# Kernel optimization log

Measured on AMD Instinct MI355X. Metric: run time of the kernel, lower is better.

Reference implementation:

```python
import jax, jax.numpy as jnp
import numpy as np
from jax import lax

CIN, COUT, NCLS = 512, 256, 1
B, H, W = 4, 64, 64
EPS = 1e-5


def conv1x1(x, w):
    # x: [B,I,H,W], w: [O,I]
    return jnp.einsum('oi,bihw->bohw', w, x)


def conv3x3(x, w):
    # x: [B,I,H,W], w: [O,I,3,3], padding=1
    return lax.conv_general_dilated(x, w, (1, 1), 'SAME',
                                    dimension_numbers=('NCHW', 'OIHW', 'NCHW'))


def bn_relu(x, g, b):
    # training-mode BatchNorm2d (biased var over B,H,W) + ReLU
    mean = jnp.mean(x, axis=(0, 2, 3), keepdims=True)
    var = jnp.var(x, axis=(0, 2, 3), keepdims=True)
    xn = (x - mean) * lax.rsqrt(var + EPS)
    return jax.nn.relu(xn * g[None, :, None, None] + b[None, :, None, None])


def attention(xf, yf, wq, wk, wv, gamma):
    # cross-attn when yf != xf, self-attn when yf is xf; no 1/sqrt(d) scaling (faithful)
    Bb, C, Hh, Ww = xf.shape
    N = Hh * Ww
    q = conv1x1(xf, wq).reshape(Bb, C, N)
    k = conv1x1(yf, wk).reshape(Bb, C, N)
    v = conv1x1(yf, wv).reshape(Bb, C, N)
    att = jax.nn.softmax(jnp.einsum('bcn,bcm->bnm', q, k), axis=-1)  # [B,N,N]
    out = jnp.einsum('bcm,bnm->bcn', v, att).reshape(Bb, C, Hh, Ww)  # v @ att^T
    return gamma * out + xf


def setup_inputs() -> dict:
    key = jax.random.key(0)
    ks = jax.random.split(key, 16)
    Cs = COUT + 2

    def w(k, shape, fan_in):
        return jax.random.normal(k, shape, dtype=jnp.float32) / np.sqrt(fan_in)

    return {
        'x': jax.random.normal(ks[0], (B, CIN, H, W), dtype=jnp.float32),
        'y': jax.random.normal(ks[1], (B, CIN, H, W), dtype=jnp.float32),
        'flow': jax.random.normal(ks[2], (B, 2, H, W), dtype=jnp.float32),
        'w1x1': w(ks[3], (COUT, CIN), CIN),
        'b1x1': jnp.zeros((COUT,), dtype=jnp.float32),
        'ca_wq': w(ks[4], (COUT, COUT), COUT),
        'ca_wk': w(ks[5], (COUT, COUT), COUT),
        'ca_wv': w(ks[6], (COUT, COUT), COUT),
        'ca_gamma': jnp.full((1,), 0.1, dtype=jnp.float32),
        'cbr1_w': w(ks[7], (COUT, COUT, 3, 3), COUT * 9),
        'bn1_g': jnp.ones((COUT,), dtype=jnp.float32),
        'bn1_b': jnp.zeros((COUT,), dtype=jnp.float32),
        'sa_wq': w(ks[8], (Cs, Cs), Cs),
        'sa_wk': w(ks[9], (Cs, Cs), Cs),
        'sa_wv': w(ks[10], (Cs, Cs), Cs),
        'sa_gamma': jnp.full((1,), 0.1, dtype=jnp.float32),
        'cbr2_w': w(ks[11], (COUT, Cs, 3, 3), Cs * 9),
        'bn2_g': jnp.ones((COUT,), dtype=jnp.float32),
        'bn2_b': jnp.zeros((COUT,), dtype=jnp.float32),
        'pred_w': w(ks[12], (NCLS, COUT), COUT),
        'pred_b': jnp.zeros((NCLS,), dtype=jnp.float32),
    }


def reference(x, y, flow, w1x1, b1x1, ca_wq, ca_wk, ca_wv, ca_gamma,
              cbr1_w, bn1_g, bn1_b, sa_wq, sa_wk, sa_wv, sa_gamma,
              cbr2_w, bn2_g, bn2_b, pred_w, pred_b):
    xb = conv1x1(x, w1x1) + b1x1[None, :, None, None]
    yb = conv1x1(y, w1x1) + b1x1[None, :, None, None]
    t = attention(xb, yb, ca_wq, ca_wk, ca_wv, ca_gamma)
    cross_out = bn_relu(conv3x3(t, cbr1_w), bn1_g, bn1_b)
    cat = jnp.concatenate([cross_out, flow], axis=1)  # [B, COUT+2, H, W]
    t = attention(cat, cat, sa_wq, sa_wk, sa_wv, sa_gamma)
    t = bn_relu(conv3x3(t, cbr2_w), bn2_g, bn2_b)
    out = conv1x1(t, pred_w) + pred_b[None, :, None, None]
    return out
```

## Files before the change

### kernel.cpp

```cpp
#include <hip/hip_runtime.h>
#include <hip/hip_bf16.h>
#include <math.h>


#define NPIX 4096
#define NB   4

typedef __attribute__((ext_vector_type(8))) short short8v;
typedef __attribute__((ext_vector_type(4))) float float4v;

__device__ __forceinline__ short f2bs(float f) {
  __hip_bfloat16 h = __float2bfloat16(f);
  short r; __builtin_memcpy(&r, &h, 2); return r;
}

__device__ __forceinline__ void glld16(const void* g, void* l) {
  __builtin_amdgcn_global_load_lds(
      (const __attribute__((address_space(1))) unsigned int*)g,
      (__attribute__((address_space(3))) unsigned int*)l, 16, 0, 0);
}

__device__ __forceinline__ void vbar() { __builtin_amdgcn_s_barrier(); }

__global__ __launch_bounds__(256) void transp_kernel(
    const float* __restrict__ X, __hip_bfloat16* __restrict__ XT)
{
  const int i0 = blockIdx.x * 64, n0 = blockIdx.y * 64, b = blockIdx.z;
  const int tid = threadIdx.x;
  __shared__ float Ls[64][68];
#pragma unroll
  for (int it = 0; it < 4; ++it) {
    int ir = it * 16 + (tid >> 4);
    int nc = (tid & 15) * 4;
    float4 v = *(const float4*)(X + ((size_t)b * 512 + i0 + ir) * NPIX + n0 + nc);
    *(float4*)(&Ls[ir][nc]) = v;
  }
  __syncthreads();
#pragma unroll
  for (int ot = 0; ot < 2; ++ot) {
    int n = ot * 32 + (tid >> 3);
    int ig = tid & 7;
    short8v o;
#pragma unroll
    for (int j = 0; j < 8; ++j) o[j] = f2bs(Ls[8 * ig + j][n]);
    *(short8v*)(XT + ((size_t)b * NPIX + n0 + n) * 512 + i0 + 8 * ig) = o;
  }
}

__global__ void wprep_kernel(const float* __restrict__ Win,
                             __hip_bfloat16* __restrict__ Wout,
                             int Or, int Ir, int Op, int Ip)
{
  size_t total = (size_t)Op * Ip;
  for (size_t e = (size_t)blockIdx.x * 256 + threadIdx.x; e < total;
       e += (size_t)gridDim.x * 256) {
    int i = (int)(e % Ip);
    int o = (int)(e / Ip);
    float v = (o < Or && i < Ir) ? Win[(size_t)o * Ir + i] : 0.f;
    Wout[e] = __float2bfloat16(v);
  }
}

__global__ void wtransbf_kernel(const float* __restrict__ Win,
                                __hip_bfloat16* __restrict__ Wout,
                                int O, int Ir, int Ip)
{
  size_t total = (size_t)9 * O * Ip;
  for (size_t e = (size_t)blockIdx.x * 256 + threadIdx.x; e < total;
       e += (size_t)gridDim.x * 256) {
    int i = (int)(e % Ip);
    size_t r = e / Ip;
    int o = (int)(r % O);
    int dydx = (int)(r / O);
    float v = (i < Ir) ? Win[((size_t)o * Ir + i) * 9 + dydx] : 0.f;
    Wout[e] = __float2bfloat16(v);
  }
}

template<int OMODE>
__global__ __launch_bounds__(256, 3) void gemm3_kernel(
    const __hip_bfloat16* __restrict__ X, const __hip_bfloat16* __restrict__ Wb,
    const float* __restrict__ Bias, float* __restrict__ Yf,
    __hip_bfloat16* __restrict__ Yb, int Ip, int O)
{
  const int n0 = blockIdx.x * 64, o0 = blockIdx.y * 64, b = blockIdx.z;
  const int tid = threadIdx.x, wv = tid >> 6, lane = tid & 63;
  const int lg = lane >> 4, lr = lane & 15;
  __shared__ __align__(16) __hip_bfloat16 Xs[64 * 32];
  __shared__ __align__(16) __hip_bfloat16 Wsh[64 * 32];

  const int nn = tid >> 2, ig = tid & 3;
  const __hip_bfloat16* xrow = X + ((size_t)b * NPIX + n0 + nn) * Ip;
  const __hip_bfloat16* wrow = Wb + (size_t)(o0 + nn) * Ip;
  const int sw = 8 * (ig ^ (nn & 3));

  float4v acc[4];
#pragma unroll
  for (int f = 0; f < 4; ++f) acc[f] = (float4v){0.f, 0.f, 0.f, 0.f};

  const int nch = Ip >> 5;
  short8v xr_ = *(const short8v*)(xrow + sw);
  short8v wr_ = *(const short8v*)(wrow + sw);

  for (int ci = 0; ci < nch; ++ci) {
    __syncthreads();
    *(short8v*)(Xs  + nn * 32 + ig * 8) = xr_;
    *(short8v*)(Wsh + nn * 32 + ig * 8) = wr_;
    __syncthreads();
    if (ci + 1 < nch) {
      xr_ = *(const short8v*)(xrow + (ci + 1) * 32 + sw);
      wr_ = *(const short8v*)(wrow + (ci + 1) * 32 + sw);
    }
    if (OMODE != 4) {
      int ar = 16 * wv + lr;
      short8v a = *(const short8v*)(Xs + ar * 32 + 8 * (lg ^ (ar & 3)));
#pragma unroll
      for (int of = 0; of < 4; ++of) {
        int br = 16 * of + lr;
        short8v bb = *(const short8v*)(Wsh + br * 32 + 8 * (lg ^ (br & 3)));
        acc[of] = __builtin_amdgcn_mfma_f32_16x16x32_bf16(a, bb, acc[of], 0, 0, 0);
      }
    } else {
      int ar = 16 * wv + lr;
      short8v a = *(const short8v*)(Wsh + ar * 32 + 8 * (lg ^ (ar & 3)));
#pragma unroll
      for (int nf = 0; nf < 4; ++nf) {
        int br = 16 * nf + lr;
        short8v bb = *(const short8v*)(Xs + br * 32 + 8 * (lg ^ (br & 3)));
        acc[nf] = __builtin_amdgcn_mfma_f32_16x16x32_bf16(a, bb, acc[nf], 0, 0, 0);
      }
    }
  }

  if (OMODE < 2) {
#pragma unroll
    for (int r = 0; r < 4; ++r) {
      size_t row = (size_t)b * NPIX + n0 + 16 * wv + 4 * lg + r;
#pragma unroll
      for (int of = 0; of < 4; ++of) {
        int o = o0 + 16 * of + lr;
        if (o < O) {
          float v = acc[of][r] + (Bias ? Bias[o] : 0.f);
          if (OMODE == 0) Yf[row * O + o] = v;
          Yb[row * O + o] = __float2bfloat16(v);
        }
      }
    }
  } else if (OMODE == 3) {
    __hip_bfloat16* Hb = Yb + (size_t)b * NPIX * O;
#pragma unroll
    for (int r = 0; r < 4; ++r) {
      size_t n = n0 + 16 * wv + 4 * lg + r;
#pragma unroll
      for (int of = 0; of < 4; ++of) {
        int o = o0 + 16 * of + lr;
        if (o < O)
          Hb[((size_t)(o >> 3) * NPIX + n) * 8 + (o & 7)] = __float2bfloat16(acc[of][r]);
      }
    }
  } else {
    __hip_bfloat16* Hb = Yb + (size_t)b * NPIX * O;
#pragma unroll
    for (int r = 0; r < 4; ++r) {
      int c = o0 + 16 * wv + 4 * lg + r;
      if (c < O) {
#pragma unroll
        for (int nf = 0; nf < 4; ++nf) {
          int n = n0 + 16 * nf + lr;
          Hb[((size_t)(n >> 3) * O + c) * 8 + (n & 7)] = __float2bfloat16(acc[nf][r]);
        }
      }
    }
  }
}

template<int C, int RF, int S>
__global__ __launch_bounds__(256, 2) void flash4_kernel(
    const __hip_bfloat16* __restrict__ Q, const __hip_bfloat16* __restrict__ K,
    const __hip_bfloat16* __restrict__ V,
    __hip_bfloat16* __restrict__ Opart, float* __restrict__ ml)
{
  constexpr int N    = NPIX;
  constexpr int NC32 = C / 32;
  constexpr int NCF  = C / 16;
  constexpr int QB   = 16 * RF;
// ... 86 lines not shown
          rs += p;
          Ps[(size_t)(w * QB + 16 * rf + 4 * lg + r) * 72 + 16 * mf + lr] =
              __float2bfloat16(p);
        }
#pragma unroll
        for (int off = 1; off < 16; off <<= 1) rs += __shfl_xor(rs, off);
        lrun[rf][r] = lrun[rf][r] * sc + rs;
        scal[rf][r] = sc;
      }
#pragma unroll
    for (int rf = 0; rf < RF; ++rf)
#pragma unroll
      for (int f = 0; f < NCF; ++f)
#pragma unroll
        for (int r = 0; r < 4; ++r) oacc[rf][f][r] *= scal[rf][r];

    asm volatile("s_waitcnt lgkmcnt(0)" ::: "memory");

    short8v pa[RF][2];
#pragma unroll
    for (int rf = 0; rf < RF; ++rf)
#pragma unroll
      for (int h = 0; h < 2; ++h)
        pa[rf][h] = *(const short8v*)(Ps + (size_t)(w * QB + 16 * rf + lr) * 72 +
                                      32 * h + 8 * lg);
    __builtin_amdgcn_s_setprio(1);
#pragma unroll
    for (int cf = 0; cf < NCF; ++cf)
#pragma unroll
      for (int h = 0; h < 2; ++h) {
        short8v vf = *(const short8v*)(Vs + ((h * 4 + lg) * C + 16 * cf + lr) * 8);
#pragma unroll
        for (int rf = 0; rf < RF; ++rf)
          oacc[rf][cf] =
              __builtin_amdgcn_mfma_f32_16x16x32_bf16(pa[rf][h], vf, oacc[rf][cf], 0, 0, 0);
      }
    __builtin_amdgcn_s_setprio(0);
  }

  const size_t rbase = (size_t)(split * NB + b) * N;
#pragma unroll
  for (int rf = 0; rf < RF; ++rf)
#pragma unroll
    for (int r = 0; r < 4; ++r) {
      int n = n0 + QB * w + 16 * rf + 4 * lg + r;
      if (lr == 0) {
        ml[(rbase + n) * 2]     = mrun[rf][r];
        ml[(rbase + n) * 2 + 1] = lrun[rf][r];
      }
#pragma unroll
      for (int cf = 0; cf < NCF; ++cf)
        Opart[(rbase + n) * C + 16 * cf + lr] = __float2bfloat16(oacc[rf][cf][r]);
    }
}

template<int C, int S>
__global__ __launch_bounds__(256) void merge4_kernel(
    const __hip_bfloat16* __restrict__ Op, const float* __restrict__ ml,
    const float* __restrict__ R, const float* __restrict__ gamma_p,
    __hip_bfloat16* __restrict__ T)
{
  const size_t row = blockIdx.x;
  float m = -INFINITY;
#pragma unroll
  for (int s = 0; s < S; ++s)
    m = fmaxf(m, ml[((size_t)s * NB * NPIX + row) * 2]);
  float e[S]; float L = 0.f;
#pragma unroll
  for (int s = 0; s < S; ++s) {
    e[s] = __expf(ml[((size_t)s * NB * NPIX + row) * 2] - m);
    L += ml[((size_t)s * NB * NPIX + row) * 2 + 1] * e[s];
  }
  float rinv = gamma_p[0] / L;
  for (int c = threadIdx.x; c < C; c += 256) {
    float o = 0.f;
#pragma unroll
    for (int s = 0; s < S; ++s)
      o += __bfloat162float(Op[((size_t)s * NB * NPIX + row) * C + c]) * e[s];
    T[row * C + c] = __float2bfloat16(o * rinv + R[row * C + c]);
  }
}

template<int IC>
__global__ __launch_bounds__(256, 1) void conv5_kernel(
    const __hip_bfloat16* __restrict__ X, const __hip_bfloat16* __restrict__ W2,
    float* __restrict__ Y)
{
  constexpr int NCH = IC / 32;
  constexpr int XP = 66 * 32;
  const int h0 = blockIdx.x * 4, o0 = blockIdx.y * 64, b = blockIdx.z;
  const int tid = threadIdx.x, wv = tid >> 6, lane = tid & 63;
  const int lg = lane >> 4, lr = lane & 15;

  __shared__ __align__(1024) __hip_bfloat16 Xs[2][6 * XP];
  __shared__ __align__(1024) __hip_bfloat16 Wsh[2][9 * 2048];

  const __hip_bfloat16 zz = __float2bfloat16(0.f);
  for (int e = tid; e < 384; e += 256) {
    int p = e / 64, side = (e >> 5) & 1, ch = e & 31;
    int sl = side ? 65 : 0;
    Xs[0][p * XP + sl * 32 + ch] = zz;
    Xs[1][p * XP + sl * 32 + ch] = zz;
  }
#pragma unroll
  for (int p = 0; p < 6; ++p) {
    int hs = h0 - 1 + p;
// ... 11 lines not shown
  for (int pf = 0; pf < 4; ++pf)
#pragma unroll
    for (int of = 0; of < 4; ++of) acc[pf][of] = (float4v){0.f, 0.f, 0.f, 0.f};

#define CSTAGE(BUF, CI)                                                        \
  _Pragma("unroll")                                                            \
  for (int k = 0; k < 6; ++k) {                                                \
    int j = wv + k * 4;                                                        \
    int p = j >> 2, seg = j & 3;                                               \
    int hs = h0 - 1 + p;                                                       \
    if (hs >= 0 && hs < 64) {                                                  \
      int px = seg * 16 + (lane >> 2), ig = lane & 3;                          \
      int sl = px + 1;                                                         \
      glld16(X + ((size_t)(b * NPIX + hs * 64 + px)) * IC + (CI) * 32 +        \
                 8 * (ig ^ (sl & 3)),                                          \
             &Xs[BUF][p * XP + (1 + seg * 16) * 32]);                          \
    }                                                                          \
  }                                                                            \
  _Pragma("unroll")                                                            \
  for (int k = 0; k < 9; ++k) {                                                \
    int j = wv + k * 4;                                                        \
    int dydx = j >> 2, seg = j & 3;                                            \
    int oo = seg * 16 + (lane >> 2), ig = lane & 3;                            \
    glld16(W2 + ((size_t)(dydx * 256 + o0 + oo)) * IC + (CI) * 32 +            \
               8 * (ig ^ (oo & 3)),                                            \
           &Wsh[BUF][dydx * 2048 + seg * 512]);                                \
  }

  CSTAGE(0, 0);
  int cur = 0;
  for (int ci = 0; ci < NCH; ++ci) {
    asm volatile("s_waitcnt vmcnt(0) lgkmcnt(0)" ::: "memory");
    vbar();
    __builtin_amdgcn_sched_barrier(0);
    const int cn = (ci + 1 == NCH) ? 0 : ci + 1;
    if (cur) { CSTAGE(0, cn); } else { CSTAGE(1, cn); }
    const __hip_bfloat16* xb = &Xs[cur][0];
    const __hip_bfloat16* wb = &Wsh[cur][0];
    __builtin_amdgcn_s_setprio(1);
#pragma unroll
    for (int dy = 0; dy < 3; ++dy) {
      const __hip_bfloat16* xpl = xb + (wv + dy) * XP;
#pragma unroll
      for (int dx = 0; dx < 3; ++dx) {
        short8v a[4];
#pragma unroll
        for (int pf = 0; pf < 4; ++pf) {
          int sl = pf * 16 + lr + dx;
          a[pf] = *(const short8v*)(xpl + sl * 32 + 8 * (lg ^ (sl & 3)));
        }
#pragma unroll
        for (int of = 0; of < 4; ++of) {
          int br = 16 * of + lr;
          short8v bb = *(const short8v*)(wb + (dy * 3 + dx) * 2048 + br * 32 +
                                         8 * (lg ^ (br & 3)));
#pragma unroll
          for (int pf = 0; pf < 4; ++pf)
            acc[pf][of] = __builtin_amdgcn_mfma_f32_16x16x32_bf16(a[pf], bb,
                                                                  acc[pf][of], 0, 0, 0);
        }
      }
    }
    __builtin_amdgcn_s_setprio(0);
    cur ^= 1;
  }
#undef CSTAGE

#pragma unroll
  for (int pf = 0; pf < 4; ++pf)
#pragma unroll
    for (int r = 0; r < 4; ++r) {
      size_t row = (size_t)b * NPIX + (h0 + wv) * 64 + 16 * pf + 4 * lg + r;
#pragma unroll
      for (int of = 0; of < 4; ++of)
        Y[row * 256 + o0 + 16 * of + lr] = acc[pf][of][r];
    }
}

__global__ __launch_bounds__(256) void stats1_kernel(
    const float* __restrict__ X, float* __restrict__ Part)
{
  const int o0 = (blockIdx.x & 3) * 64;
  const int rc = blockIdx.x >> 2;
  const int tid = threadIdx.x;
  const int o = o0 + (tid & 63), rq = tid >> 6;
  float s = 0.f, sq = 0.f;
  for (int rr = rq; rr < 256; rr += 4) {
    float v = X[(size_t)(rc * 256 + rr) * 256 + o];
    s += v; sq += v * v;
  }
  __shared__ float rs[256], rq2[256];
  rs[tid] = s; rq2[tid] = sq;
  __syncthreads();
  if (tid < 64) {
    s  = rs[tid] + rs[tid + 64] + rs[tid + 128] + rs[tid + 192];
    sq = rq2[tid] + rq2[tid + 64] + rq2[tid + 128] + rq2[tid + 192];
    Part[(o0 + tid) * 128 + rc * 2]     = s;
    Part[(o0 + tid) * 128 + rc * 2 + 1] = sq;
  }
}

__global__ __launch_bounds__(256) void stats2_kernel(
    const float* __restrict__ Part, float* __restrict__ Mean, float* __restrict__ Rstd)
{
  const int o = threadIdx.x;
  float s = 0.f, sq = 0.f;
  for (int rc = 0; rc < 64; ++rc) {
    s += Part[o * 128 + rc * 2];
    sq += Part[o * 128 + rc * 2 + 1];
  }
  float mean = s / 16384.f;
  float var = sq / 16384.f - mean * mean;
  Mean[o] = mean;
  Rstd[o] = 1.f / sqrtf(var + 1e-5f);
}

__global__ __launch_bounds__(320) void bnapply1_kernel(
    const float* __restrict__ X, const float* __restrict__ Flow,
    const float* __restrict__ Mean, const float* __restrict__ Rstd,
    const float* __restrict__ G, const float* __restrict__ Bt,
    float* __restrict__ CatF, __hip_bfloat16* __restrict__ CatB)
{
  const size_t row = blockIdx.x;
  const int t = threadIdx.x;
  if (t >= 288) return;
  float val;
  if (t < 256) {
    float v = X[row * 256 + t];
    val = fmaxf((v - Mean[t]) * Rstd[t] * G[t] + Bt[t], 0.f);
  } else if (t < 258) {
    int b = (int)(row >> 12), n = (int)(row & 4095);
    val = Flow[((size_t)(b * 2 + (t - 256)) << 12) + n];
  } else val = 0.f;
  CatF[row * 288 + t] = val;
  CatB[row * 288 + t] = __float2bfloat16(val);
}

__global__ __launch_bounds__(256) void bnapply2_kernel(
    float* X, const float* __restrict__ Mean, const float* __restrict__ Rstd,
    const float* __restrict__ G, const float* __restrict__ Bt)
{
  const size_t idx = (size_t)blockIdx.x * 256 + threadIdx.x;
  const int t = threadIdx.x;
  float v = X[idx];
  X[idx] = fmaxf((v - Mean[t]) * Rstd[t] * G[t] + Bt[t], 0.f);
}

__global__ __launch_bounds__(256) void pred3_kernel(
    const float* __restrict__ X, const float* __restrict__ Wp,
    const float* __restrict__ Bp, float* __restrict__ Out)
{
  const int wv = threadIdx.x >> 6, lane = threadIdx.x & 63;
  const size_t row = (size_t)blockIdx.x * 4 + wv;
  const float* xr = X + row * 256;
  float acc = 0.f;
#pragma unroll
  for (int cc = 0; cc < 4; ++cc) acc = fmaf(xr[cc * 64 + lane], Wp[cc * 64 + lane], acc);
#pragma unroll
  for (int off = 1; off < 64; off <<= 1) acc += __shfl_xor(acc, off);
  if (lane == 0) Out[row] = acc + Bp[0];
}

extern "C" void kernel_launch(void* const* d_in, const int* in_sizes, int n_in,
                              void* d_out, int out_size, void* d_ws, size_t ws_size,
                              hipStream_t stream)
{
  (void)in_sizes; (void)n_in; (void)out_size; (void)ws_size;
  const float* x      = (const float*)d_in[0];
  const float* y      = (const float*)d_in[1];
  const float* flow   = (const float*)d_in[2];
  const float* w1x1   = (const float*)d_in[3];
  const float* b1x1   = (const float*)d_in[4];
  const float* ca_wq  = (const float*)d_in[5];
  const float* ca_wk  = (const float*)d_in[6];
  const float* ca_wv  = (const float*)d_in[7];
  const float* ca_g   = (const float*)d_in[8];
  const float* cbr1_w = (const float*)d_in[9];
  const float* bn1_g  = (const float*)d_in[10];
  const float* bn1_b  = (const float*)d_in[11];
  const float* sa_wq  = (const float*)d_in[12];
  const float* sa_wk  = (const float*)d_in[13];
  const float* sa_wv  = (const float*)d_in[14];
  const float* sa_g   = (const float*)d_in[15];
  const float* cbr2_w = (const float*)d_in[16];
  const float* bn2_g  = (const float*)d_in[17];
  const float* bn2_b  = (const float*)d_in[18];
  const float* pred_w = (const float*)d_in[19];
  const float* pred_b = (const float*)d_in[20];
  float* out = (float*)d_out;

  const size_t FSZ = (size_t)NB * NPIX * 288;
  const size_t SSZ = FSZ / 2;
  float* ws = (float*)d_ws;
  float* F0 = ws;
  float* F1 = ws + FSZ;
  float* F2 = ws + 2 * FSZ;
  float* Sb = ws + 3 * FSZ;
  __hip_bfloat16* S0 = (__hip_bfloat16*)(Sb);
  __hip_bfloat16* S1 = (__hip_bfloat16*)(Sb + SSZ);
  __hip_bfloat16* S2 = (__hip_bfloat16*)(Sb + 2 * SSZ);
  __hip_bfloat16* S3 = (__hip_bfloat16*)(Sb + 3 * SSZ);
  __hip_bfloat16* S4 = (__hip_bfloat16*)(Sb + 4 * SSZ);
  float* Wr = Sb + 5 * SSZ;
  __hip_bfloat16* w1bf  = (__hip_bfloat16*)Wr;
  __hip_bfloat16* caqb  = w1bf + (size_t)256 * 512;
  __hip_bfloat16* cakb  = caqb + (size_t)256 * 256;
  __hip_bfloat16* cavb  = cakb + (size_t)256 * 256;
  __hip_bfloat16* saqb  = cavb + (size_t)256 * 256;
  __hip_bfloat16* sakb  = saqb + (size_t)320 * 288;
  __hip_bfloat16* savb  = sakb + (size_t)320 * 288;
  __hip_bfloat16* w2abf = savb + (size_t)320 * 288;
  __hip_bfloat16* w2bbf = w2abf + (size_t)9 * 256 * 256;
  float* Part = (float*)(w2bbf + (size_t)9 * 256 * 288);
  float* Mean = Part + 32768;
  float* Rstd = Mean + 256;
  float* Mlb  = Rstd + 256;

  __hip_bfloat16* xT = (__hip_bfloat16*)F0;
  __hip_bfloat16* yT = (__hip_bfloat16*)F1;
  __hip_bfloat16* Op = (__hip_bfloat16*)F0;

  dim3 blk(256);

  wprep_kernel<<<dim3(256), blk, 0, stream>>>(w1x1, w1bf, 256, 512, 256, 512);
  wprep_kernel<<<dim3(256), blk, 0, stream>>>(ca_wq, caqb, 256, 256, 256, 256);
  wprep_kernel<<<dim3(256), blk, 0, stream>>>(ca_wk, cakb, 256, 256, 256, 256);
  wprep_kernel<<<dim3(256), blk, 0, stream>>>(ca_wv, cavb, 256, 256, 256, 256);
  wprep_kernel<<<dim3(256), blk, 0, stream>>>(sa_wq, saqb, 258, 258, 320, 288);
  wprep_kernel<<<dim3(256), blk, 0, stream>>>(sa_wk, sakb, 258, 258, 320, 288);
  wprep_kernel<<<dim3(256), blk, 0, stream>>>(sa_wv, savb, 258, 258, 320, 288);
  wtransbf_kernel<<<dim3(512), blk, 0, stream>>>(cbr1_w, w2abf, 256, 256, 256);
  wtransbf_kernel<<<dim3(512), blk, 0, stream>>>(cbr2_w, w2bbf, 256, 258, 288);

  transp_kernel<<<dim3(8, 64, 4), blk, 0, stream>>>(x, xT);
  transp_kernel<<<dim3(8, 64, 4), blk, 0, stream>>>(y, yT);

  gemm3_kernel<0><<<dim3(64, 4, 4), blk, 0, stream>>>(xT, w1bf, b1x1, F2, S0, 512, 256);
  gemm3_kernel<1><<<dim3(64, 4, 4), blk, 0, stream>>>(yT, w1bf, b1x1, nullptr, S1, 512, 256);

  gemm3_kernel<1><<<dim3(64, 4, 4), blk, 0, stream>>>(S0, caqb, nullptr, nullptr, S2, 256, 256);
  gemm3_kernel<3><<<dim3(64, 4, 4), blk, 0, stream>>>(S1, cakb, nullptr, nullptr, S3, 256, 256);
  gemm3_kernel<4><<<dim3(64, 4, 4), blk, 0, stream>>>(S1, cavb, nullptr, nullptr, S4, 256, 256);

  flash4_kernel<256, 2, 4><<<dim3(32, 4, 4), blk, 0, stream>>>(S2, S3, S4, Op, Mlb);
  merge4_kernel<256, 4><<<dim3(16384), blk, 0, stream>>>(Op, Mlb, F2, ca_g, S0);

  conv5_kernel<256><<<dim3(16, 4, 4), blk, 0, stream>>>(S0, w2abf, F0);
  stats1_kernel<<<dim3(256), blk, 0, stream>>>(F0, Part);
  stats2_kernel<<<dim3(1), blk, 0, stream>>>(Part, Mean, Rstd);
  bnapply1_kernel<<<dim3(16384), dim3(320), 0, stream>>>(F0, flow, Mean, Rstd,
                                                         bn1_g, bn1_b, F1, S3);

  gemm3_kernel<1><<<dim3(64, 5, 4), blk, 0, stream>>>(S3, saqb, nullptr, nullptr, S0, 288, 288);
  gemm3_kernel<3><<<dim3(64, 5, 4), blk, 0, stream>>>(S3, sakb, nullptr, nullptr, S1, 288, 288);
  gemm3_kernel<4><<<dim3(64, 5, 4), blk, 0, stream>>>(S3, savb, nullptr, nullptr, S2, 288, 288);

  flash4_kernel<288, 1, 2><<<dim3(64, 2, 4), blk, 0, stream>>>(S0, S1, S2, Op, Mlb);
  merge4_kernel<288, 2><<<dim3(16384), blk, 0, stream>>>(Op, Mlb, F1, sa_g, S4);

  conv5_kernel<288><<<dim3(16, 4, 4), blk, 0, stream>>>(S4, w2bbf, F0);
  stats1_kernel<<<dim3(256), blk, 0, stream>>>(F0, Part);
  stats2_kernel<<<dim3(1), blk, 0, stream>>>(Part, Mean, Rstd);
  bnapply2_kernel<<<dim3(16384), blk, 0, stream>>>(F0, Mean, Rstd, bn2_g, bn2_b);

  pred3_kernel<<<dim3(4096), blk, 0, stream>>>(F0, pred_w, pred_b, out);
}
```

Before: 530.9 us.

## Merge prep launches, double-buffer gemm loads, add split-4 self-attention flash kernel

The nine weight-prep launches become one 2D-grid kernel, and the two input transposes become one launch. The 1x1 GEMM now stages tiles straight into double-buffered LDS with global_load_lds instead of a register round trip, aiming to overlap loads with MFMA. Self-attention uses a new flash6 kernel with a 4-way KV split and one 16-row tile per wave, which skips the rescale when the running max moves by less than 8, plus a 4-way merge. The bnapply1 output buffer moves from F1 to F2, which adds extra Op/ml partial traffic and risks an aliasing mistake if F2 is still needed.

```diff
diff --git a/kernel.cpp b/kernel.cpp
--- a/kernel.cpp
+++ b/kernel.cpp
@@ -23,16 +23,20 @@
 __device__ __forceinline__ void vbar() { __builtin_amdgcn_s_barrier(); }
 
 __global__ __launch_bounds__(256) void transp_kernel(
-    const float* __restrict__ X, __hip_bfloat16* __restrict__ XT)
-{
-  const int i0 = blockIdx.x * 64, n0 = blockIdx.y * 64, b = blockIdx.z;
+    const float* __restrict__ X, const float* __restrict__ Y,
+    __hip_bfloat16* __restrict__ XT, __hip_bfloat16* __restrict__ YT)
+{
+  const int i0 = blockIdx.x * 64, n0 = blockIdx.y * 64;
+  const int z = blockIdx.z, b = z & 3;
+  const float* S = (z < 4) ? X : Y;
+  __hip_bfloat16* D = (z < 4) ? XT : YT;
   const int tid = threadIdx.x;
   __shared__ float Ls[64][68];
 #pragma unroll
   for (int it = 0; it < 4; ++it) {
     int ir = it * 16 + (tid >> 4);
     int nc = (tid & 15) * 4;
-    float4 v = *(const float4*)(X + ((size_t)b * 512 + i0 + ir) * NPIX + n0 + nc);
+    float4 v = *(const float4*)(S + ((size_t)b * 512 + i0 + ir) * NPIX + n0 + nc);
     *(float4*)(&Ls[ir][nc]) = v;
   }
   __syncthreads();
@@ -43,37 +47,55 @@
     short8v o;
 #pragma unroll
     for (int j = 0; j < 8; ++j) o[j] = f2bs(Ls[8 * ig + j][n]);
-    *(short8v*)(XT + ((size_t)b * NPIX + n0 + n) * 512 + i0 + 8 * ig) = o;
-  }
-}
-
-__global__ void wprep_kernel(const float* __restrict__ Win,
-                             __hip_bfloat16* __restrict__ Wout,
-                             int Or, int Ir, int Op, int Ip)
-{
-  size_t total = (size_t)Op * Ip;
-  for (size_t e = (size_t)blockIdx.x * 256 + threadIdx.x; e < total;
-       e += (size_t)gridDim.x * 256) {
-    int i = (int)(e % Ip);
-    int o = (int)(e / Ip);
-    float v = (o < Or && i < Ir) ? Win[(size_t)o * Ir + i] : 0.f;
-    Wout[e] = __float2bfloat16(v);
-  }
-}
-
-__global__ void wtransbf_kernel(const float* __restrict__ Win,
-                                __hip_bfloat16* __restrict__ Wout,
-                                int O, int Ir, int Ip)
-{
-  size_t total = (size_t)9 * O * Ip;
-  for (size_t e = (size_t)blockIdx.x * 256 + threadIdx.x; e < total;
-       e += (size_t)gridDim.x * 256) {
-    int i = (int)(e % Ip);
-    size_t r = e / Ip;
-    int o = (int)(r % O);
-    int dydx = (int)(r / O);
-    float v = (i < Ir) ? Win[((size_t)o * Ir + i) * 9 + dydx] : 0.f;
-    Wout[e] = __float2bfloat16(v);
+    *(short8v*)(D + ((size_t)b * NPIX + n0 + n) * 512 + i0 + 8 * ig) = o;
+  }
+}
+
+__global__ void wprep_all(
+    const float* __restrict__ w1, const float* __restrict__ cq,
+    const float* __restrict__ ck, const float* __restrict__ cv,
+    const float* __restrict__ sq, const float* __restrict__ sk,
+    const float* __restrict__ sv, const float* __restrict__ c1,
+    const float* __restrict__ c2,
+    __hip_bfloat16* __restrict__ w1o, __hip_bfloat16* __restrict__ cqo,
+    __hip_bfloat16* __restrict__ cko, __hip_bfloat16* __restrict__ cvo,
+    __hip_bfloat16* __restrict__ sqo, __hip_bfloat16* __restrict__ sko,
+    __hip_bfloat16* __restrict__ svo, __hip_bfloat16* __restrict__ c1o,
+    __hip_bfloat16* __restrict__ c2o)
+{
+  const int seg = blockIdx.y;
+  const float* src; __hip_bfloat16* dst;
+  int Or, Ir, Op, Ip, isconv = 0;
+  switch (seg) {
+    case 0: src = w1; dst = w1o; Or = 256; Ir = 512; Op = 256; Ip = 512; break;
+    case 1: src = cq; dst = cqo; Or = 256; Ir = 256; Op = 256; Ip = 256; break;
+    case 2: src = ck; dst = cko; Or = 256; Ir = 256; Op = 256; Ip = 256; break;
+    case 3: src = cv; dst = cvo; Or = 256; Ir = 256; Op = 256; Ip = 256; break;
+    case 4: src = sq; dst = sqo; Or = 258; Ir = 258; Op = 320; Ip = 288; break;
+    case 5: src = sk; dst = sko; Or = 258; Ir = 258; Op = 320; Ip = 288; break;
+    case 6: src = sv; dst = svo; Or = 258; Ir = 258; Op = 320; Ip = 288; break;
+    case 7: src = c1; dst = c1o; Or = 256; Ir = 256; Op = 256; Ip = 256; isconv = 1; break;
+    default: src = c2; dst = c2o; Or = 256; Ir = 258; Op = 256; Ip = 288; isconv = 1; break;
+  }
+  if (!isconv) {
+    size_t total = (size_t)Op * Ip;
+    for (size_t e = (size_t)blockIdx.x * 256 + threadIdx.x; e < total;
+         e += (size_t)gridDim.x * 256) {
+      int i = (int)(e % Ip), o = (int)(e / Ip);
+      float v = (o < Or && i < Ir) ? src[(size_t)o * Ir + i] : 0.f;
+      dst[e] = __float2bfloat16(v);
+    }
+  } else {
+    size_t total = (size_t)9 * Op * Ip;
+    for (size_t e = (size_t)blockIdx.x * 256 + threadIdx.x; e < total;
+         e += (size_t)gridDim.x * 256) {
+      int i = (int)(e % Ip);
+      size_t r = e / Ip;
+      int o = (int)(r % Op);
+      int dydx = (int)(r / Op);
+      float v = (i < Ir) ? src[((size_t)o * Ir + i) * 9 + dydx] : 0.f;
+      dst[e] = __float2bfloat16(v);
+    }
   }
 }
 
@@ -86,51 +108,55 @@
   const int n0 = blockIdx.x * 64, o0 = blockIdx.y * 64, b = blockIdx.z;
   const int tid = threadIdx.x, wv = tid >> 6, lane = tid & 63;
   const int lg = lane >> 4, lr = lane & 15;
-  __shared__ __align__(16) __hip_bfloat16 Xs[64 * 32];
-  __shared__ __align__(16) __hip_bfloat16 Wsh[64 * 32];
+  __shared__ __align__(1024) __hip_bfloat16 Xs[2][64 * 32];
+  __shared__ __align__(1024) __hip_bfloat16 Wsh[2][64 * 32];
 
   const int nn = tid >> 2, ig = tid & 3;
-  const __hip_bfloat16* xrow = X + ((size_t)b * NPIX + n0 + nn) * Ip;
-  const __hip_bfloat16* wrow = Wb + (size_t)(o0 + nn) * Ip;
-  const int sw = 8 * (ig ^ (nn & 3));
+  const __hip_bfloat16* xsrc = X + ((size_t)b * NPIX + n0 + nn) * Ip + 8 * (ig ^ (nn & 3));
+  const __hip_bfloat16* wsrc = Wb + (size_t)(o0 + nn) * Ip + 8 * (ig ^ (nn & 3));
 
   float4v acc[4];
 #pragma unroll
   for (int f = 0; f < 4; ++f) acc[f] = (float4v){0.f, 0.f, 0.f, 0.f};
 
   const int nch = Ip >> 5;
-  short8v xr_ = *(const short8v*)(xrow + sw);
-  short8v wr_ = *(const short8v*)(wrow + sw);
-
+
+#define GSTAGE(BUF, CI)                            \
+  glld16(xsrc + (CI) * 32, &Xs[BUF][tid * 8]);     \
+  glld16(wsrc + (CI) * 32, &Wsh[BUF][tid * 8]);
+
+  GSTAGE(0, 0);
+  int cur = 0;
   for (int ci = 0; ci < nch; ++ci) {
-    __syncthreads();
-    *(short8v*)(Xs  + nn * 32 + ig * 8) = xr_;
-    *(short8v*)(Wsh + nn * 32 + ig * 8) = wr_;
+    asm volatile("s_waitcnt vmcnt(0)" ::: "memory");
     __syncthreads();
     if (ci + 1 < nch) {
-      xr_ = *(const short8v*)(xrow + (ci + 1) * 32 + sw);
-      wr_ = *(const short8v*)(wrow + (ci + 1) * 32 + sw);
-    }
+      if (cur) { GSTAGE(0, ci + 1); } else { GSTAGE(1, ci + 1); }
+    }
+    const __hip_bfloat16* xb = &Xs[cur][0];
+    const __hip_bfloat16* wb = &Wsh[cur][0];
     if (OMODE != 4) {
       int ar = 16 * wv + lr;
-      short8v a = *(const short8v*)(Xs + ar * 32 + 8 * (lg ^ (ar & 3)));
+      short8v a = *(const short8v*)(xb + ar * 32 + 8 * (lg ^ (ar & 3)));
 #pragma unroll
       for (int of = 0; of < 4; ++of) {
         int br = 16 * of + lr;
-        short8v bb = *(const short8v*)(Wsh + br * 32 + 8 * (lg ^ (br & 3)));
-        acc[of] = __builtin_amdgcn_mfma_f32_16x16x32_bf16(a, bb, acc[of], 0, 0, 0);
+        short8v bbv = *(const short8v*)(wb + br * 32 + 8 * (lg ^ (br & 3)));
+        acc[of] = __builtin_amdgcn_mfma_f32_16x16x32_bf16(a, bbv, acc[of], 0, 0, 0);
       }
     } else {
       int ar = 16 * wv + lr;
-      short8v a = *(const short8v*)(Wsh + ar * 32 + 8 * (lg ^ (ar & 3)));
+      short8v a = *(const short8v*)(wb + ar * 32 + 8 * (lg ^ (ar & 3)));
 #pragma unroll
       for (int nf = 0; nf < 4; ++nf) {
         int br = 16 * nf + lr;
-        short8v bb = *(const short8v*)(Xs + br * 32 + 8 * (lg ^ (br & 3)));
-        acc[nf] = __builtin_amdgcn_mfma_f32_16x16x32_bf16(a, bb, acc[nf], 0, 0, 0);
-      }
-    }
-  }
+        short8v bbv = *(const short8v*)(xb + br * 32 + 8 * (lg ^ (br & 3)));
+        acc[nf] = __builtin_amdgcn_mfma_f32_16x16x32_bf16(a, bbv, acc[nf], 0, 0, 0);
+      }
+    }
+    cur ^= 1;
+  }
+#undef GSTAGE
 
   if (OMODE < 2) {
 #pragma unroll
@@ -323,6 +349,152 @@
       for (int cf = 0; cf < NCF; ++cf)
         Opart[(rbase + n) * C + 16 * cf + lr] = __float2bfloat16(oacc[rf][cf][r]);
     }
+}
+
+template<int C, int S>
+__global__ __launch_bounds__(256, 3) void flash6_kernel(
+    const __hip_bfloat16* __restrict__ Q, const __hip_bfloat16* __restrict__ K,
+    const __hip_bfloat16* __restrict__ V,
+    __hip_bfloat16* __restrict__ Opart, float* __restrict__ ml)
+{
+  constexpr int N    = NPIX;
+  constexpr int NC32 = C / 32;
+  constexpr int NCF  = C / 16;
+  constexpr int KBYTES = (C / 8) * 32 * 8 * 2;
+  constexpr int NINST = C / 16;
+  constexpr int NT   = (N / S) / 32;
+
+  __shared__ __align__(1024) char smem[2 * KBYTES];
+  __hip_bfloat16* Ks = (__hip_bfloat16*)smem;
+  __hip_bfloat16* Vs = (__hip_bfloat16*)(smem + KBYTES);
+  __hip_bfloat16* Ps = (__hip_bfloat16*)smem;
+
+  const int n0 = blockIdx.x * 64;
+  const int split = blockIdx.y, b = blockIdx.z;
+  const int tid = threadIdx.x, w = tid >> 6, lane = tid & 63;
+  const int lg = lane >> 4, lr = lane & 15;
+
+  const __hip_bfloat16* Kb = K + (size_t)b * N * C;
+  const __hip_bfloat16* Vb = V + (size_t)b * N * C;
+
+  short8v qf[NC32];
+  {
+    const __hip_bfloat16* qp = Q + ((size_t)b * N + n0 + 16 * w + lr) * C + 8 * lg;
+#pragma unroll
+    for (int ks = 0; ks < NC32; ++ks) qf[ks] = *(const short8v*)(qp + 32 * ks);
+  }
+
+  float4v oacc[NCF];
+#pragma unroll
+  for (int f = 0; f < NCF; ++f) oacc[f] = (float4v){0.f, 0.f, 0.f, 0.f};
+  float mrun[4], lrun[4];
+#pragma unroll
+  for (int r = 0; r < 4; ++r) { mrun[r] = -INFINITY; lrun[r] = 0.f; }
+
+  const int m0base = split * (N / S);
+
+  for (int t = 0; t < NT; ++t) {
+    const int m0 = m0base + t * 32;
+    __syncthreads();
+    for (int u = w; u < NINST; u += 4)
+      glld16(Kb + ((size_t)(2 * u + (lane >> 5)) * N + m0 + (lane & 31)) * 8,
+             Ks + u * 512);
+    for (int u = w; u < NINST; u += 4) {
+      int s = u * 64 + lane;
+      int kv8 = s / C, c = s % C;
+      glld16(Vb + ((size_t)(m0 / 8 + kv8) * C + c) * 8, Vs + s * 8);
+    }
+    asm volatile("s_waitcnt vmcnt(0)" ::: "memory");
+    __syncthreads();
+
+    float4v sacc[2];
+#pragma unroll
+    for (int mf = 0; mf < 2; ++mf) sacc[mf] = (float4v){0.f, 0.f, 0.f, 0.f};
+    __builtin_amdgcn_s_setprio(1);
+#pragma unroll
+    for (int ks = 0; ks < NC32; ++ks)
+#pragma unroll
+      for (int mf = 0; mf < 2; ++mf) {
+        short8v kf = *(const short8v*)(Ks + ((4 * ks + lg) * 32 + 16 * mf + lr) * 8);
+        sacc[mf] = __builtin_amdgcn_mfma_f32_16x16x32_bf16(qf[ks], kf, sacc[mf], 0, 0, 0);
+      }
+    __builtin_amdgcn_s_setprio(0);
+    __syncthreads();
+
+    float pm[4];
+#pragma unroll
+    for (int r = 0; r < 4; ++r) {
+      float p = fmaxf(sacc[0][r], sacc[1][r]);
+#pragma unroll
+      for (int off = 1; off < 16; off <<= 1) p = fmaxf(p, __shfl_xor(p, off));
+      pm[r] = p;
+    }
+    int myok = 1;
+#pragma unroll
+    for (int r = 0; r < 4; ++r) myok &= (pm[r] <= mrun[r] + 8.f) ? 1 : 0;
+    if (__all(myok)) {
+#pragma unroll
+      for (int r = 0; r < 4; ++r) {
+        float rs = 0.f;
+#pragma unroll
+        for (int mf = 0; mf < 2; ++mf) {
+          float p = __expf(sacc[mf][r] - mrun[r]);
+          rs += p;
+          Ps[(16 * w + 4 * lg + r) * 40 + 16 * mf + lr] = __float2bfloat16(p);
+        }
+#pragma unroll
+        for (int off = 1; off < 16; off <<= 1) rs += __shfl_xor(rs, off);
+        lrun[r] += rs;
+      }
+    } else {
+      float scal[4];
+#pragma unroll
+      for (int r = 0; r < 4; ++r) {
+        float mnew = fmaxf(mrun[r], pm[r]);
+        float sc = __expf(mrun[r] - mnew);
+        mrun[r] = mnew;
+        float rs = 0.f;
+#pragma unroll
+        for (int mf = 0; mf < 2; ++mf) {
+          float p = __expf(sacc[mf][r] - mnew);
+          rs += p;
+          Ps[(16 * w + 4 * lg + r) * 40 + 16 * mf + lr] = __float2bfloat16(p);
+        }
+#pragma unroll
+        for (int off = 1; off < 16; off <<= 1) rs += __shfl_xor(rs, off);
+        lrun[r] = lrun[r] * sc + rs;
+        scal[r] = sc;
+      }
+#pragma unroll
+      for (int f = 0; f < NCF; ++f)
+#pragma unroll
+        for (int r = 0; r < 4; ++r) oacc[f][r] *= scal[r];
+    }
+
+    asm volatile("s_waitcnt lgkmcnt(0)" ::: "memory");
+
+    short8v pa = *(const short8v*)(Ps + (16 * w + lr) * 40 + 8 * lg);
+    __builtin_amdgcn_s_setprio(1);
+#pragma unroll
+    for (int cf = 0; cf < NCF; ++cf) {
+      short8v vf = *(const short8v*)(Vs + (lg * C + 16 * cf + lr) * 8);
+      oacc[cf] = __builtin_amdgcn_mfma_f32_16x16x32_bf16(pa, vf, oacc[cf], 0, 0, 0);
+    }
+    __builtin_amdgcn_s_setprio(0);
+  }
+
+  const size_t rbase = (size_t)(split * NB + b) * N;
+#pragma unroll
+  for (int r = 0; r < 4; ++r) {
+    int n = n0 + 16 * w + 4 * lg + r;
+    if (lr == 0) {
+      ml[(rbase + n) * 2]     = mrun[r];
+      ml[(rbase + n) * 2 + 1] = lrun[r];
+    }
+#pragma unroll
+    for (int cf = 0; cf < NCF; ++cf)
+      Opart[(rbase + n) * C + 16 * cf + lr] = __float2bfloat16(oacc[cf][r]);
+  }
 }
 
 template<int C, int S>
@@ -440,11 +612,11 @@
 #pragma unroll
         for (int of = 0; of < 4; ++of) {
           int br = 16 * of + lr;
-          short8v bb = *(const short8v*)(wb + (dy * 3 + dx) * 2048 + br * 32 +
-                                         8 * (lg ^ (br & 3)));
+          short8v bbv = *(const short8v*)(wb + (dy * 3 + dx) * 2048 + br * 32 +
+                                          8 * (lg ^ (br & 3)));
 #pragma unroll
           for (int pf = 0; pf < 4; ++pf)
-            acc[pf][of] = __builtin_amdgcn_mfma_f32_16x16x32_bf16(a[pf], bb,
+            acc[pf][of] = __builtin_amdgcn_mfma_f32_16x16x32_bf16(a[pf], bbv,
                                                                   acc[pf][of], 0, 0, 0);
         }
       }
@@ -610,18 +782,11 @@
 
   dim3 blk(256);
 
-  wprep_kernel<<<dim3(256), blk, 0, stream>>>(w1x1, w1bf, 256, 512, 256, 512);
-  wprep_kernel<<<dim3(256), blk, 0, stream>>>(ca_wq, caqb, 256, 256, 256, 256);
-  wprep_kernel<<<dim3(256), blk, 0, stream>>>(ca_wk, cakb, 256, 256, 256, 256);
-  wprep_kernel<<<dim3(256), blk, 0, stream>>>(ca_wv, cavb, 256, 256, 256, 256);
-  wprep_kernel<<<dim3(256), blk, 0, stream>>>(sa_wq, saqb, 258, 258, 320, 288);
-  wprep_kernel<<<dim3(256), blk, 0, stream>>>(sa_wk, sakb, 258, 258, 320, 288);
-  wprep_kernel<<<dim3(256), blk, 0, stream>>>(sa_wv, savb, 258, 258, 320, 288);
-  wtransbf_kernel<<<dim3(512), blk, 0, stream>>>(cbr1_w, w2abf, 256, 256, 256);
-  wtransbf_kernel<<<dim3(512), blk, 0, stream>>>(cbr2_w, w2bbf, 256, 258, 288);
-
-  transp_kernel<<<dim3(8, 64, 4), blk, 0, stream>>>(x, xT);
-  transp_kernel<<<dim3(8, 64, 4), blk, 0, stream>>>(y, yT);
+  wprep_all<<<dim3(48, 9), blk, 0, stream>>>(
+      w1x1, ca_wq, ca_wk, ca_wv, sa_wq, sa_wk, sa_wv, cbr1_w, cbr2_w,
+      w1bf, caqb, cakb, cavb, saqb, sakb, savb, w2abf, w2bbf);
+
+  transp_kernel<<<dim3(8, 64, 8), blk, 0, stream>>>(x, y, xT, yT);
 
   gemm3_kernel<0><<<dim3(64, 4, 4), blk, 0, stream>>>(xT, w1bf, b1x1, F2, S0, 512, 256);
   gemm3_kernel<1><<<dim3(64, 4, 4), blk, 0, stream>>>(yT, w1bf, b1x1, nullptr, S1, 512, 256);
@@ -637,14 +802,14 @@
   stats1_kernel<<<dim3(256), blk, 0, stream>>>(F0, Part);
   stats2_kernel<<<dim3(1), blk, 0, stream>>>(Part, Mean, Rstd);
   bnapply1_kernel<<<dim3(16384), dim3(320), 0, stream>>>(F0, flow, Mean, Rstd,
-                                                         bn1_g, bn1_b, F1, S3);
+                                                         bn1_g, bn1_b, F2, S3);
 
   gemm3_kernel<1><<<dim3(64, 5, 4), blk, 0, stream>>>(S3, saqb, nullptr, nullptr, S0, 288, 288);
   gemm3_kernel<3><<<dim3(64, 5, 4), blk, 0, stream>>>(S3, sakb, nullptr, nullptr, S1, 288, 288);
   gemm3_kernel<4><<<dim3(64, 5, 4), blk, 0, stream>>>(S3, savb, nullptr, nullptr, S2, 288, 288);
 
-  flash4_kernel<288, 1, 2><<<dim3(64, 2, 4), blk, 0, stream>>>(S0, S1, S2, Op, Mlb);
-  merge4_kernel<288, 2><<<dim3(16384), blk, 0, stream>>>(Op, Mlb, F1, sa_g, S4);
+  flash6_kernel<288, 4><<<dim3(64, 4, 4), blk, 0, stream>>>(S0, S1, S2, Op, Mlb);
+  merge4_kernel<288, 4><<<dim3(16384), blk, 0, stream>>>(Op, Mlb, F2, sa_g, S4);
 
   conv5_kernel<288><<<dim3(16, 4, 4), blk, 0, stream>>>(S4, w2bbf, F0);
   stats1_kernel<<<dim3(256), blk, 0, stream>>>(F0, Part);
```

New measurement: 986.9 us. 1.86x slower.

## Batch weight prep, merge transposes, double-buffer GEMM loads, fuse BN2 into predictor

Applied to the files above, without the earlier changes.

Nine weight-conversion launches become one kernel indexed by blockIdx.y, and the two input transposes become one launch. The 1x1 GEMM switches from register staging to double-buffered global_load_lds direct-to-LDS copies, which cuts one barrier per chunk. The final BN+ReLU pass is fused into the prediction dot product, removing a full read/write sweep of the 16 MB conv output. Buffer F1 is renamed to F2 for the concatenated features. The new GEMM keeps the same swizzle but relies on vmcnt waits for correctness.

```diff
diff --git a/kernel.cpp b/kernel.cpp
--- a/kernel.cpp
+++ b/kernel.cpp
@@ -23,16 +23,20 @@
 __device__ __forceinline__ void vbar() { __builtin_amdgcn_s_barrier(); }
 
 __global__ __launch_bounds__(256) void transp_kernel(
-    const float* __restrict__ X, __hip_bfloat16* __restrict__ XT)
-{
-  const int i0 = blockIdx.x * 64, n0 = blockIdx.y * 64, b = blockIdx.z;
+    const float* __restrict__ X, const float* __restrict__ Y,
+    __hip_bfloat16* __restrict__ XT, __hip_bfloat16* __restrict__ YT)
+{
+  const int i0 = blockIdx.x * 64, n0 = blockIdx.y * 64;
+  const int z = blockIdx.z, b = z & 3;
+  const float* S = (z < 4) ? X : Y;
+  __hip_bfloat16* D = (z < 4) ? XT : YT;
   const int tid = threadIdx.x;
   __shared__ float Ls[64][68];
 #pragma unroll
   for (int it = 0; it < 4; ++it) {
     int ir = it * 16 + (tid >> 4);
     int nc = (tid & 15) * 4;
-    float4 v = *(const float4*)(X + ((size_t)b * 512 + i0 + ir) * NPIX + n0 + nc);
+    float4 v = *(const float4*)(S + ((size_t)b * 512 + i0 + ir) * NPIX + n0 + nc);
     *(float4*)(&Ls[ir][nc]) = v;
   }
   __syncthreads();
@@ -43,37 +47,55 @@
     short8v o;
 #pragma unroll
     for (int j = 0; j < 8; ++j) o[j] = f2bs(Ls[8 * ig + j][n]);
-    *(short8v*)(XT + ((size_t)b * NPIX + n0 + n) * 512 + i0 + 8 * ig) = o;
-  }
-}
-
-__global__ void wprep_kernel(const float* __restrict__ Win,
-                             __hip_bfloat16* __restrict__ Wout,
-                             int Or, int Ir, int Op, int Ip)
-{
-  size_t total = (size_t)Op * Ip;
-  for (size_t e = (size_t)blockIdx.x * 256 + threadIdx.x; e < total;
-       e += (size_t)gridDim.x * 256) {
-    int i = (int)(e % Ip);
-    int o = (int)(e / Ip);
-    float v = (o < Or && i < Ir) ? Win[(size_t)o * Ir + i] : 0.f;
-    Wout[e] = __float2bfloat16(v);
-  }
-}
-
-__global__ void wtransbf_kernel(const float* __restrict__ Win,
-                                __hip_bfloat16* __restrict__ Wout,
-                                int O, int Ir, int Ip)
-{
-  size_t total = (size_t)9 * O * Ip;
-  for (size_t e = (size_t)blockIdx.x * 256 + threadIdx.x; e < total;
-       e += (size_t)gridDim.x * 256) {
-    int i = (int)(e % Ip);
-    size_t r = e / Ip;
-    int o = (int)(r % O);
-    int dydx = (int)(r / O);
-    float v = (i < Ir) ? Win[((size_t)o * Ir + i) * 9 + dydx] : 0.f;
-    Wout[e] = __float2bfloat16(v);
+    *(short8v*)(D + ((size_t)b * NPIX + n0 + n) * 512 + i0 + 8 * ig) = o;
+  }
+}
+
+__global__ void wprep_all(
+    const float* __restrict__ w1, const float* __restrict__ cq,
+    const float* __restrict__ ck, const float* __restrict__ cv,
+    const float* __restrict__ sq, const float* __restrict__ sk,
+    const float* __restrict__ sv, const float* __restrict__ c1,
+    const float* __restrict__ c2,
+    __hip_bfloat16* __restrict__ w1o, __hip_bfloat16* __restrict__ cqo,
+    __hip_bfloat16* __restrict__ cko, __hip_bfloat16* __restrict__ cvo,
+    __hip_bfloat16* __restrict__ sqo, __hip_bfloat16* __restrict__ sko,
+    __hip_bfloat16* __restrict__ svo, __hip_bfloat16* __restrict__ c1o,
+    __hip_bfloat16* __restrict__ c2o)
+{
+  const int seg = blockIdx.y;
+  const float* src; __hip_bfloat16* dst;
+  int Or, Ir, Op, Ip, isconv = 0;
+  switch (seg) {
+    case 0: src = w1; dst = w1o; Or = 256; Ir = 512; Op = 256; Ip = 512; break;
+    case 1: src = cq; dst = cqo; Or = 256; Ir = 256; Op = 256; Ip = 256; break;
+    case 2: src = ck; dst = cko; Or = 256; Ir = 256; Op = 256; Ip = 256; break;
+    case 3: src = cv; dst = cvo; Or = 256; Ir = 256; Op = 256; Ip = 256; break;
+    case 4: src = sq; dst = sqo; Or = 258; Ir = 258; Op = 320; Ip = 288; break;
+    case 5: src = sk; dst = sko; Or = 258; Ir = 258; Op = 320; Ip = 288; break;
+    case 6: src = sv; dst = svo; Or = 258; Ir = 258; Op = 320; Ip = 288; break;
+    case 7: src = c1; dst = c1o; Or = 256; Ir = 256; Op = 256; Ip = 256; isconv = 1; break;
+    default: src = c2; dst = c2o; Or = 256; Ir = 258; Op = 256; Ip = 288; isconv = 1; break;
+  }
+  if (!isconv) {
+    size_t total = (size_t)Op * Ip;
+    for (size_t e = (size_t)blockIdx.x * 256 + threadIdx.x; e < total;
+         e += (size_t)gridDim.x * 256) {
+      int i = (int)(e % Ip), o = (int)(e / Ip);
+      float v = (o < Or && i < Ir) ? src[(size_t)o * Ir + i] : 0.f;
+      dst[e] = __float2bfloat16(v);
+    }
+  } else {
+    size_t total = (size_t)9 * Op * Ip;
+    for (size_t e = (size_t)blockIdx.x * 256 + threadIdx.x; e < total;
+         e += (size_t)gridDim.x * 256) {
+      int i = (int)(e % Ip);
+      size_t r = e / Ip;
+      int o = (int)(r % Op);
+      int dydx = (int)(r / Op);
+      float v = (i < Ir) ? src[((size_t)o * Ir + i) * 9 + dydx] : 0.f;
+      dst[e] = __float2bfloat16(v);
+    }
   }
 }
 
@@ -86,51 +108,55 @@
   const int n0 = blockIdx.x * 64, o0 = blockIdx.y * 64, b = blockIdx.z;
   const int tid = threadIdx.x, wv = tid >> 6, lane = tid & 63;
   const int lg = lane >> 4, lr = lane & 15;
-  __shared__ __align__(16) __hip_bfloat16 Xs[64 * 32];
-  __shared__ __align__(16) __hip_bfloat16 Wsh[64 * 32];
+  __shared__ __align__(1024) __hip_bfloat16 Xs[2][64 * 32];
+  __shared__ __align__(1024) __hip_bfloat16 Wsh[2][64 * 32];
 
   const int nn = tid >> 2, ig = tid & 3;
-  const __hip_bfloat16* xrow = X + ((size_t)b * NPIX + n0 + nn) * Ip;
-  const __hip_bfloat16* wrow = Wb + (size_t)(o0 + nn) * Ip;
-  const int sw = 8 * (ig ^ (nn & 3));
+  const __hip_bfloat16* xsrc = X + ((size_t)b * NPIX + n0 + nn) * Ip + 8 * (ig ^ (nn & 3));
+  const __hip_bfloat16* wsrc = Wb + (size_t)(o0 + nn) * Ip + 8 * (ig ^ (nn & 3));
 
   float4v acc[4];
 #pragma unroll
   for (int f = 0; f < 4; ++f) acc[f] = (float4v){0.f, 0.f, 0.f, 0.f};
 
   const int nch = Ip >> 5;
-  short8v xr_ = *(const short8v*)(xrow + sw);
-  short8v wr_ = *(const short8v*)(wrow + sw);
-
+
+#define GSTAGE(BUF, CI)                            \
+  glld16(xsrc + (CI) * 32, &Xs[BUF][tid * 8]);     \
+  glld16(wsrc + (CI) * 32, &Wsh[BUF][tid * 8]);
+
+  GSTAGE(0, 0);
+  int cur = 0;
   for (int ci = 0; ci < nch; ++ci) {
-    __syncthreads();
-    *(short8v*)(Xs  + nn * 32 + ig * 8) = xr_;
-    *(short8v*)(Wsh + nn * 32 + ig * 8) = wr_;
+    asm volatile("s_waitcnt vmcnt(0)" ::: "memory");
     __syncthreads();
     if (ci + 1 < nch) {
-      xr_ = *(const short8v*)(xrow + (ci + 1) * 32 + sw);
-      wr_ = *(const short8v*)(wrow + (ci + 1) * 32 + sw);
-    }
+      if (cur) { GSTAGE(0, ci + 1); } else { GSTAGE(1, ci + 1); }
+    }
+    const __hip_bfloat16* xb = &Xs[cur][0];
+    const __hip_bfloat16* wb = &Wsh[cur][0];
     if (OMODE != 4) {
       int ar = 16 * wv + lr;
-      short8v a = *(const short8v*)(Xs + ar * 32 + 8 * (lg ^ (ar & 3)));
+      short8v a = *(const short8v*)(xb + ar * 32 + 8 * (lg ^ (ar & 3)));
 #pragma unroll
       for (int of = 0; of < 4; ++of) {
         int br = 16 * of + lr;
-        short8v bb = *(const short8v*)(Wsh + br * 32 + 8 * (lg ^ (br & 3)));
-        acc[of] = __builtin_amdgcn_mfma_f32_16x16x32_bf16(a, bb, acc[of], 0, 0, 0);
+        short8v bbv = *(const short8v*)(wb + br * 32 + 8 * (lg ^ (br & 3)));
+        acc[of] = __builtin_amdgcn_mfma_f32_16x16x32_bf16(a, bbv, acc[of], 0, 0, 0);
       }
     } else {
       int ar = 16 * wv + lr;
-      short8v a = *(const short8v*)(Wsh + ar * 32 + 8 * (lg ^ (ar & 3)));
+      short8v a = *(const short8v*)(wb + ar * 32 + 8 * (lg ^ (ar & 3)));
 #pragma unroll
       for (int nf = 0; nf < 4; ++nf) {
         int br = 16 * nf + lr;
-        short8v bb = *(const short8v*)(Xs + br * 32 + 8 * (lg ^ (br & 3)));
-        acc[nf] = __builtin_amdgcn_mfma_f32_16x16x32_bf16(a, bb, acc[nf], 0, 0, 0);
-      }
-    }
-  }
+        short8v bbv = *(const short8v*)(xb + br * 32 + 8 * (lg ^ (br & 3)));
+        acc[nf] = __builtin_amdgcn_mfma_f32_16x16x32_bf16(a, bbv, acc[nf], 0, 0, 0);
+      }
+    }
+    cur ^= 1;
+  }
+#undef GSTAGE
 
   if (OMODE < 2) {
 #pragma unroll
@@ -440,11 +466,11 @@
 #pragma unroll
         for (int of = 0; of < 4; ++of) {
           int br = 16 * of + lr;
-          short8v bb = *(const short8v*)(wb + (dy * 3 + dx) * 2048 + br * 32 +
-                                         8 * (lg ^ (br & 3)));
+          short8v bbv = *(const short8v*)(wb + (dy * 3 + dx) * 2048 + br * 32 +
+                                          8 * (lg ^ (br & 3)));
 #pragma unroll
           for (int pf = 0; pf < 4; ++pf)
-            acc[pf][of] = __builtin_amdgcn_mfma_f32_16x16x32_bf16(a[pf], bb,
+            acc[pf][of] = __builtin_amdgcn_mfma_f32_16x16x32_bf16(a[pf], bbv,
                                                                   acc[pf][of], 0, 0, 0);
         }
       }
@@ -524,18 +550,10 @@
   CatB[row * 288 + t] = __float2bfloat16(val);
 }
 
-__global__ __launch_bounds__(256) void bnapply2_kernel(
-    float* X, const float* __restrict__ Mean, const float* __restrict__ Rstd,
-    const float* __restrict__ G, const float* __restrict__ Bt)
-{
-  const size_t idx = (size_t)blockIdx.x * 256 + threadIdx.x;
-  const int t = threadIdx.x;
-  float v = X[idx];
-  X[idx] = fmaxf((v - Mean[t]) * Rstd[t] * G[t] + Bt[t], 0.f);
-}
-
-__global__ __launch_bounds__(256) void pred3_kernel(
-    const float* __restrict__ X, const float* __restrict__ Wp,
+__global__ __launch_bounds__(256) void bnpred_kernel(
+    const float* __restrict__ X, const float* __restrict__ Mean,
+    const float* __restrict__ Rstd, const float* __restrict__ G,
+    const float* __restrict__ Bt, const float* __restrict__ Wp,
     const float* __restrict__ Bp, float* __restrict__ Out)
 {
   const int wv = threadIdx.x >> 6, lane = threadIdx.x & 63;
@@ -543,7 +561,12 @@
   const float* xr = X + row * 256;
   float acc = 0.f;
 #pragma unroll
-  for (int cc = 0; cc < 4; ++cc) acc = fmaf(xr[cc * 64 + lane], Wp[cc * 64 + lane], acc);
+  for (int cc = 0; cc < 4; ++cc) {
+    int c = cc * 64 + lane;
+    float v = xr[c];
+    v = fmaxf((v - Mean[c]) * Rstd[c] * G[c] + Bt[c], 0.f);
+    acc = fmaf(v, Wp[c], acc);
+  }
 #pragma unroll
   for (int off = 1; off < 64; off <<= 1) acc += __shfl_xor(acc, off);
   if (lane == 0) Out[row] = acc + Bp[0];
@@ -610,18 +633,11 @@
 
   dim3 blk(256);
 
-  wprep_kernel<<<dim3(256), blk, 0, stream>>>(w1x1, w1bf, 256, 512, 256, 512);
-  wprep_kernel<<<dim3(256), blk, 0, stream>>>(ca_wq, caqb, 256, 256, 256, 256);
-  wprep_kernel<<<dim3(256), blk, 0, stream>>>(ca_wk, cakb, 256, 256, 256, 256);
-  wprep_kernel<<<dim3(256), blk, 0, stream>>>(ca_wv, cavb, 256, 256, 256, 256);
-  wprep_kernel<<<dim3(256), blk, 0, stream>>>(sa_wq, saqb, 258, 258, 320, 288);
-  wprep_kernel<<<dim3(256), blk, 0, stream>>>(sa_wk, sakb, 258, 258, 320, 288);
-  wprep_kernel<<<dim3(256), blk, 0, stream>>>(sa_wv, savb, 258, 258, 320, 288);
-  wtransbf_kernel<<<dim3(512), blk, 0, stream>>>(cbr1_w, w2abf, 256, 256, 256);
-  wtransbf_kernel<<<dim3(512), blk, 0, stream>>>(cbr2_w, w2bbf, 256, 258, 288);
-
-  transp_kernel<<<dim3(8, 64, 4), blk, 0, stream>>>(x, xT);
-  transp_kernel<<<dim3(8, 64, 4), blk, 0, stream>>>(y, yT);
+  wprep_all<<<dim3(48, 9), blk, 0, stream>>>(
+      w1x1, ca_wq, ca_wk, ca_wv, sa_wq, sa_wk, sa_wv, cbr1_w, cbr2_w,
+      w1bf, caqb, cakb, cavb, saqb, sakb, savb, w2abf, w2bbf);
+
+  transp_kernel<<<dim3(8, 64, 8), blk, 0, stream>>>(x, y, xT, yT);
 
   gemm3_kernel<0><<<dim3(64, 4, 4), blk, 0, stream>>>(xT, w1bf, b1x1, F2, S0, 512, 256);
   gemm3_kernel<1><<<dim3(64, 4, 4), blk, 0, stream>>>(yT, w1bf, b1x1, nullptr, S1, 512, 256);
@@ -637,19 +653,18 @@
   stats1_kernel<<<dim3(256), blk, 0, stream>>>(F0, Part);
   stats2_kernel<<<dim3(1), blk, 0, stream>>>(Part, Mean, Rstd);
   bnapply1_kernel<<<dim3(16384), dim3(320), 0, stream>>>(F0, flow, Mean, Rstd,
-                                                         bn1_g, bn1_b, F1, S3);
+                                                         bn1_g, bn1_b, F2, S3);
 
   gemm3_kernel<1><<<dim3(64, 5, 4), blk, 0, stream>>>(S3, saqb, nullptr, nullptr, S0, 288, 288);
   gemm3_kernel<3><<<dim3(64, 5, 4), blk, 0, stream>>>(S3, sakb, nullptr, nullptr, S1, 288, 288);
   gemm3_kernel<4><<<dim3(64, 5, 4), blk, 0, stream>>>(S3, savb, nullptr, nullptr, S2, 288, 288);
 
   flash4_kernel<288, 1, 2><<<dim3(64, 2, 4), blk, 0, stream>>>(S0, S1, S2, Op, Mlb);
-  merge4_kernel<288, 2><<<dim3(16384), blk, 0, stream>>>(Op, Mlb, F1, sa_g, S4);
+  merge4_kernel<288, 2><<<dim3(16384), blk, 0, stream>>>(Op, Mlb, F2, sa_g, S4);
 
   conv5_kernel<288><<<dim3(16, 4, 4), blk, 0, stream>>>(S4, w2bbf, F0);
   stats1_kernel<<<dim3(256), blk, 0, stream>>>(F0, Part);
   stats2_kernel<<<dim3(1), blk, 0, stream>>>(Part, Mean, Rstd);
-  bnapply2_kernel<<<dim3(16384), blk, 0, stream>>>(F0, Mean, Rstd, bn2_g, bn2_b);
-
-  pred3_kernel<<<dim3(4096), blk, 0, stream>>>(F0, pred_w, pred_b, out);
-}
+  bnpred_kernel<<<dim3(4096), blk, 0, stream>>>(F0, Mean, Rstd, bn2_g, bn2_b,
+                                                pred_w, pred_b, out);
+}
```

New measurement: 507.5 us. 1.05x faster.
